# Performance work log

Measured on AMD Instinct MI355X. Metric: run time of the kernel, lower is better.

The kernel has to match this reference:

```python
import jax, jax.numpy as jnp
import numpy as np

B, S, D, H = 2, 1024, 1024, 16
DK, DV = 64, 64
E, F, K = 8, 2048, 2
FSH = 2 * F  # n_shared_experts * moe_inter_dim


def layernorm(x, w, eps=1e-8):
    # RMSNormLayer actually calls F.layer_norm(x, [dim], weight, None, eps)
    mu = jnp.mean(x, axis=-1, keepdims=True)
    var = jnp.mean((x - mu) ** 2, axis=-1, keepdims=True)
    return (x - mu) * jax.lax.rsqrt(var + eps) * w


def _forward(start_pos, x, mask, pos_embedding, attn_norm_w, ffn_norm_w,
             wq, bq, wk, bk, wv, bv, wo, bo, gate_w, gate_b,
             ew1, eb1, ew2, eb2, ew3, eb3, sw1, sb1, sw2, sb2, sw3, sb3):
    b, s, d = x.shape
    # --- attention sublayer ---
    xn = layernorm(x, attn_norm_w)
    q = (xn @ wq + bq).reshape(b, s, H, DK)
    k = (xn @ wk + bk).reshape(b, s, H, DK)
    v = (xn @ wv + bv).reshape(b, s, H, DV)
    score = jnp.einsum('bshk,bShk->bhsS', q, k) / np.float32(np.sqrt(DK))
    pe = pos_embedding[:, start_pos:start_pos + s, start_pos:start_pos + s]  # [H,s,s]
    score = score + pe[None, :, :, :] + mask[:s, :s]
    attn = jax.nn.softmax(score, axis=-1)
    o = jnp.einsum('bhsS,bShv->bshv', attn, v).reshape(b, s, H * DV)
    x = x + o @ wo + bo
    # --- MoE sublayer (eval-path math: y[t] = sum_k w[t,k]*expert_{idx[t,k]}(x[t])) ---
    hn = layernorm(x, ffn_norm_w)
    flat = hn.reshape(-1, d)  # [T, D]
    logits = flat @ gate_w.T + gate_b
    scores = jax.nn.softmax(logits, axis=-1)
    topk_w, topk_idx = jax.lax.top_k(scores, K)
    topk_w = topk_w / (jnp.sum(topk_w, axis=-1, keepdims=True) + 1e-20)
    # per-token per-expert combine weight [T, E]
    comb = jnp.sum(jax.nn.one_hot(topk_idx, E, dtype=flat.dtype) * topk_w[..., None], axis=1)
    # all experts densely (small E), SwiGLU per expert
    a = jnp.einsum('td,edf->tef', flat, ew1) + eb1
    g = jnp.einsum('td,edf->tef', flat, ew3) + eb3
    mid = jax.nn.silu(a) * g
    ye = jnp.einsum('tef,efd->ted', mid, ew2) + eb2  # [T, E, D]
    y = jnp.einsum('te,ted->td', comb, ye)
    # shared experts MLP on the normed input
    shared = (jax.nn.silu(flat @ sw1 + sb1) * (flat @ sw3 + sb3)) @ sw2 + sb2
    return x + (y + shared).reshape(b, s, d)


def setup_inputs() -> dict:
    key = jax.random.key(0)
    ks = jax.random.split(key, 16)
    def rn(i, shape, s=0.02):
        return jax.random.normal(ks[i], shape, jnp.float32) * s
    return dict(
        x=rn(0, (B, S, D), 1.0),
        start_pos=0,
        mask=jnp.zeros((S, S), jnp.float32),
        pos_embedding=rn(1, (H, S, S)),
        attn_norm_w=jnp.ones((D,), jnp.float32),
        ffn_norm_w=jnp.ones((D,), jnp.float32),
        wq=rn(2, (D, H * DK)), bq=jnp.zeros((H * DK,), jnp.float32),
        wk=rn(3, (D, H * DK)), bk=jnp.zeros((H * DK,), jnp.float32),
        wv=rn(4, (D, H * DV)), bv=jnp.zeros((H * DV,), jnp.float32),
        wo=rn(5, (H * DV, D)), bo=jnp.zeros((D,), jnp.float32),
        gate_w=rn(6, (E, D), 1.0), gate_b=rn(7, (E,), 1.0),
        ew1=rn(8, (E, D, F)), eb1=jnp.zeros((E, F), jnp.float32),
        ew2=rn(9, (E, F, D)), eb2=jnp.zeros((E, D), jnp.float32),
        ew3=rn(10, (E, D, F)), eb3=jnp.zeros((E, F), jnp.float32),
        sw1=rn(11, (D, FSH)), sb1=jnp.zeros((FSH,), jnp.float32),
        sw2=rn(12, (FSH, D)), sb2=jnp.zeros((D,), jnp.float32),
        sw3=rn(13, (D, FSH)), sb3=jnp.zeros((FSH,), jnp.float32),
    )


def reference(x, start_pos, mask, pos_embedding, attn_norm_w, ffn_norm_w,
              wq, bq, wk, bk, wv, bv, wo, bo, gate_w, gate_b,
              ew1, eb1, ew2, eb2, ew3, eb3, sw1, sb1, sw2, sb2, sw3, sb3):
    return _forward(start_pos, x, mask, pos_embedding, attn_norm_w, ffn_norm_w,
                    wq, bq, wk, bk, wv, bv, wo, bo, gate_w, gate_b,
                    ew1, eb1, ew2, eb2, ew3, eb3, sw1, sb1, sw2, sb2, sw3, sb3)
```

## Files before the change

### kernel.cpp

```cpp
#include <hip/hip_runtime.h>
#include <hip/hip_bf16.h>

#define BB 2
#define SS 1024
#define DD 1024
#define HH 16
#define DKV 64
#define EE 8
#define FF 2048
#define FSH2 4096

typedef __attribute__((ext_vector_type(8))) short bf16x8;
typedef __attribute__((ext_vector_type(4))) float f32x4;

#define EPI_PLAIN 0
#define EPI_SCATTER 2
#define AM_DENSE 0
#define AM_GATHER 1
#define AM_GROUP 2

__device__ inline unsigned pack_bf2(float lo, float hi) {
    __hip_bfloat162 h = __float22bfloat162_rn(float2{lo, hi});
    union { __hip_bfloat162 h2; unsigned u; } c; c.h2 = h; return c.u;
}
__device__ inline unsigned short bf16_1(float x) {
    union { __hip_bfloat16 b; unsigned short u; } c;
    c.b = __float2bfloat16(x); return c.u;
}

#define LOADT(s, k0) {                                                        \
    const float4* ap4 = (const float4*)(Ap + (k0));                           \
    pa##s##_0 = ap4[0]; pa##s##_1 = ap4[1];                                   \
    pa##s##_2 = ap4[2]; pa##s##_3 = ap4[3];                                   \
    const float* wp = Wcol + (size_t)((k0) + kg * 8) * N;                     \
    _Pragma("unroll")                                                         \
    for (int j = 0; j < 8; ++j) pb##s[j] = wp[(size_t)j * N];                 \
}
#define STAGET(s) {                                                           \
    uint4 aw0, aw1;                                                           \
    aw0.x = pack_bf2(pa##s##_0.x, pa##s##_0.y);                               \
    aw0.y = pack_bf2(pa##s##_0.z, pa##s##_0.w);                               \
    aw0.z = pack_bf2(pa##s##_1.x, pa##s##_1.y);                               \
    aw0.w = pack_bf2(pa##s##_1.z, pa##s##_1.w);                               \
    aw1.x = pack_bf2(pa##s##_2.x, pa##s##_2.y);                               \
    aw1.y = pack_bf2(pa##s##_2.z, pa##s##_2.w);                               \
    aw1.z = pack_bf2(pa##s##_3.x, pa##s##_3.y);                               \
    aw1.w = pack_bf2(pa##s##_3.z, pa##s##_3.w);                               \
    *(uint4*)&As[ar * 40 + ac] = aw0;                                         \
    *(uint4*)&As[ar * 40 + ac + 8] = aw1;                                     \
    uint4 bw;                                                                 \
    bw.x = pack_bf2(pb##s[0], pb##s[1]);  bw.y = pack_bf2(pb##s[2], pb##s[3]);\
    bw.z = pack_bf2(pb##s[4], pb##s[5]);  bw.w = pack_bf2(pb##s[6], pb##s[7]);\
    *(uint4*)&Bs[bn * 32 + slB * 8] = bw;                                     \
}
#define MFMAT() {                                                             \
    bf16x8 af[4], bfr[2];                                                     \
    _Pragma("unroll")                                                         \
    for (int m = 0; m < 4; ++m) {                                             \
        int row = wr * 64 + m * 16 + ll;                                      \
        af[m] = *(const bf16x8*)&As[row * 40 + lh * 8];                       \
    }                                                                         \
    _Pragma("unroll")                                                         \
    for (int n = 0; n < 2; ++n) {                                             \
        int col = wc * 32 + n * 16 + ll;                                      \
        int slot = lh ^ (col & 3);                                            \
        bfr[n] = *(const bf16x8*)&Bs[col * 32 + slot * 8];                    \
    }                                                                         \
    _Pragma("unroll")                                                         \
    for (int m = 0; m < 4; ++m)                                               \
        _Pragma("unroll")                                                     \
        for (int n = 0; n < 2; ++n)                                           \
            acc[m][n] = __builtin_amdgcn_mfma_f32_16x16x32_bf16(af[m], bfr[n], acc[m][n], 0, 0, 0); \
}
#define PHASET(s, nx) {                                                       \
    STAGET(s)                                                                 \
    if ((nx) < NT) LOADT(s, (nx) << 5)                                        \
    asm volatile("s_waitcnt lgkmcnt(0)\n\ts_barrier" ::: "memory");           \
    MFMAT()                                                                   \
    asm volatile("s_barrier" ::: "memory");                                   \
}

template<int EPI, int AMODE, int NSEL, int SPLITK>
__global__ __launch_bounds__(256, 2) void mgemm(
    const float* __restrict__ A,
    const float* __restrict__ W0, const float* __restrict__ W1p, const float* __restrict__ W2p,
    const float* __restrict__ b0, const float* __restrict__ b1p, const float* __restrict__ b2p,
    const float* __restrict__ addsrc,
    float* __restrict__ C0, float* __restrict__ C1p, float* __restrict__ C2p,
    int M, int N, int K,
    const int* __restrict__ tok_list, const int* __restrict__ cnt,
    const int* __restrict__ offs, const float* __restrict__ comb,
    const int* __restrict__ idx0, float* __restrict__ y1)
{
    __shared__ __align__(16) unsigned short As[128 * 40];
    __shared__ __align__(16) unsigned short Bs[64 * 32];
    __shared__ int rows_s[128];
    const int t = threadIdx.x;
    const float* W = W0; const float* bias = b0; float* C = C0;
    if (NSEL == 3) {
        if (blockIdx.z == 1) { W = W1p; bias = b1p; C = C1p; }
        else if (blockIdx.z == 2) { W = W2p; bias = b2p; C = C2p; }
    }
    const int e = (AMODE != AM_DENSE) ? blockIdx.z : 0;
    int ne = M, base = 0;
    if (AMODE != AM_DENSE) {
        ne = cnt[e];
        base = offs[e];
        if ((int)blockIdx.y * 128 >= ne) return;
        W += (size_t)e * K * N;
        bias += (size_t)e * N;
    }
    const int m0 = blockIdx.y * 128;
    const int n0 = blockIdx.x * 64;
    if (AMODE == AM_GATHER) {
        if (t < 128) {
            int li = m0 + t; if (li >= ne) li = ne - 1;
            rows_s[t] = tok_list[e * 2048 + li];
        }
        __syncthreads();
    }
    const int ar = t >> 1;
    const int ac = (t & 1) * 16;
    const int bn = t & 63;
    const int kg = t >> 6;
    const int slB = kg ^ (bn & 3);
    long arow;
    if (AMODE == AM_DENSE) arow = m0 + ar;
    else if (AMODE == AM_GATHER) arow = rows_s[ar];
    else { int li = m0 + ar; if (li >= ne) li = ne - 1; arow = base + li; }
    const int Kc = (SPLITK > 1) ? (K / SPLITK) : K;
    const size_t koff = (SPLITK > 1) ? (size_t)blockIdx.z * Kc : 0;
    const float* Ap = A + (size_t)arow * K + ac + koff;
    const float* Wcol = W + koff * N + n0 + bn;
    const int l = t & 63, w = t >> 6;
    const int wr = w >> 1, wc = w & 1;
    const int lh = l >> 4, ll = l & 15;
    f32x4 acc[4][2];
#pragma unroll
    for (int i = 0; i < 4; ++i)
#pragma unroll
        for (int j = 0; j < 2; ++j) acc[i][j] = f32x4{0.f, 0.f, 0.f, 0.f};

    const int NT = Kc >> 5;
    float4 pa0_0, pa0_1, pa0_2, pa0_3; float pb0[8];
    float4 pa1_0, pa1_1, pa1_2, pa1_3; float pb1[8];
    float4 pa2_0, pa2_1, pa2_2, pa2_3; float pb2[8];
    float4 pa3_0, pa3_1, pa3_2, pa3_3; float pb3[8];
    LOADT(0, 0)
    LOADT(1, 32)
    LOADT(2, 64)
    LOADT(3, 96)
    for (int it = 0; it < NT; it += 4) {
        PHASET(0, it + 4)
        PHASET(1, it + 5)
        PHASET(2, it + 6)
        PHASET(3, it + 7)
    }

#pragma unroll
    for (int m = 0; m < 4; ++m) {
#pragma unroll
        for (int n = 0; n < 2; ++n) {
            int colg = n0 + wc * 32 + n * 16 + ll;
            float bvv = (SPLITK > 1) ? 0.f : bias[colg];
#pragma unroll
            for (int j = 0; j < 4; ++j) {
                int li = m0 + wr * 64 + m * 16 + lh * 4 + j;
                float v = acc[m][n][j] + bvv;
                if (SPLITK > 1) {
                    C[(size_t)blockIdx.z * M * N + (size_t)li * N + colg] = v;
                } else if (EPI == EPI_PLAIN) {
                    if (AMODE == AM_DENSE) {
                        if (addsrc) v += addsrc[(size_t)li * N + colg];
                        C[(size_t)li * N + colg] = v;
                    } else {
                        if (li < ne) C[(size_t)(base + li) * N + colg] = v;
                    }
                } else {
                    if (li < ne) {
                        int tok = tok_list[e * 2048 + li];
                        float wgt = comb[tok * 8 + e];
                        float* dst = (idx0[tok] == e) ? C : y1;
                        dst[(size_t)tok * N + colg] = wgt * v;
                    }
                }
            }
        }
    }
}

#define LOAD2T(s, k0) {                                                       \
    const float4* ap4 = (const float4*)(Ap + (k0));                           \
    pa##s##_0 = ap4[0]; pa##s##_1 = ap4[1];                                   \
    pa##s##_2 = ap4[2]; pa##s##_3 = ap4[3];                                   \
    const float* wp1 = W1col + (size_t)((k0) + kg * 8) * N;                   \
    const float* wp3 = W3col + (size_t)((k0) + kg * 8) * N;                   \
    _Pragma("unroll")                                                         \
    for (int j = 0; j < 8; ++j) {                                             \
        pb1##s[j] = wp1[(size_t)j * N];                                       \
        pb3##s[j] = wp3[(size_t)j * N];                                       \
    }                                                                         \
}
#define STAGE2T(s) {                                                          \
    uint4 aw0, aw1;                                                           \
    aw0.x = pack_bf2(pa##s##_0.x, pa##s##_0.y);                               \
    aw0.y = pack_bf2(pa##s##_0.z, pa##s##_0.w);                               \
    aw0.z = pack_bf2(pa##s##_1.x, pa##s##_1.y);                               \
    aw0.w = pack_bf2(pa##s##_1.z, pa##s##_1.w);                               \
    aw1.x = pack_bf2(pa##s##_2.x, pa##s##_2.y);                               \
    aw1.y = pack_bf2(pa##s##_2.z, pa##s##_2.w);                               \
    aw1.z = pack_bf2(pa##s##_3.x, pa##s##_3.y);                               \
    aw1.w = pack_bf2(pa##s##_3.z, pa##s##_3.w);                               \
    *(uint4*)&As[ar * 40 + ac] = aw0;                                         \
    *(uint4*)&As[ar * 40 + ac + 8] = aw1;                                     \
    uint4 bw;                                                                 \
    bw.x = pack_bf2(pb1##s[0], pb1##s[1]);  bw.y = pack_bf2(pb1##s[2], pb1##s[3]); \
    bw.z = pack_bf2(pb1##s[4], pb1##s[5]);  bw.w = pack_bf2(pb1##s[6], pb1##s[7]); \
    *(uint4*)&B1s[bn * 32 + slB * 8] = bw;                                    \
    bw.x = pack_bf2(pb3##s[0], pb3##s[1]);  bw.y = pack_bf2(pb3##s[2], pb3##s[3]); \
    bw.z = pack_bf2(pb3##s[4], pb3##s[5]);  bw.w = pack_bf2(pb3##s[6], pb3##s[7]); \
    *(uint4*)&B3s[bn * 32 + slB * 8] = bw;                                    \
}
#define MFMA2T() {                                                            \
    bf16x8 af[4], bfr[2];                                                     \
    _Pragma("unroll")                                                         \
    for (int m = 0; m < 4; ++m) {                                             \
        int row = wr * 64 + m * 16 + ll;                                      \
        af[m] = *(const bf16x8*)&As[row * 40 + lh * 8];                       \
    }                                                                         \
    _Pragma("unroll")                                                         \
    for (int n = 0; n < 2; ++n) {                                             \
        int col = wc * 32 + n * 16 + ll;                                      \
        int slot = lh ^ (col & 3);                                            \
        bfr[n] = *(const bf16x8*)&B1s[col * 32 + slot * 8];                   \
    }                                                                         \
    _Pragma("unroll")                                                         \
    for (int m = 0; m < 4; ++m)                                               \
        _Pragma("unroll")                                                     \
        for (int n = 0; n < 2; ++n)                                           \
            acc1[m][n] = __builtin_amdgcn_mfma_f32_16x16x32_bf16(af[m], bfr[n], acc1[m][n], 0, 0, 0); \
    _Pragma("unroll")                                                         \
    for (int n = 0; n < 2; ++n) {                                             \
        int col = wc * 32 + n * 16 + ll;                                      \
        int slot = lh ^ (col & 3);                                            \
        bfr[n] = *(const bf16x8*)&B3s[col * 32 + slot * 8];                   \
    }                                                                         \
    _Pragma("unroll")                                                         \
    for (int m = 0; m < 4; ++m)                                               \
        _Pragma("unroll")                                                     \
        for (int n = 0; n < 2; ++n)                                           \
            acc3[m][n] = __builtin_amdgcn_mfma_f32_16x16x32_bf16(af[m], bfr[n], acc3[m][n], 0, 0, 0); \
}
#define PHASE2T(s, nx) {                                                      \
    STAGE2T(s)                                                                \
    if ((nx) < NT) LOAD2T(s, (nx) << 5)                                       \
    asm volatile("s_waitcnt lgkmcnt(0)\n\ts_barrier" ::: "memory");           \
    MFMA2T()                                                                  \
    asm volatile("s_barrier" ::: "memory");                                   \
}

#define MGEMM2_BODY(GATED) {                                                  \
    const int l = t & 63, w = t >> 6;                                         \
    const int wr = w >> 1, wc = w & 1;                                        \
    const int lh = l >> 4, ll = l & 15;                                       \
    f32x4 acc1[4][2], acc3[4][2];                                             \
    _Pragma("unroll")                                                         \
    for (int i = 0; i < 4; ++i)                                               \
        _Pragma("unroll")                                                     \
        for (int j = 0; j < 2; ++j) {                                         \
            acc1[i][j] = f32x4{0.f, 0.f, 0.f, 0.f};                           \
            acc3[i][j] = f32x4{0.f, 0.f, 0.f, 0.f};                           \
        }                                                                     \
    const int NT = K >> 5;                                                    \
    float4 pa0_0, pa0_1, pa0_2, pa0_3; float pb10[8], pb30[8];                \
    float4 pa1_0, pa1_1, pa1_2, pa1_3; float pb11[8], pb31[8];                \
    LOAD2T(0, 0)                                                              \
    LOAD2T(1, 32)                                                             \
    for (int it = 0; it < NT; it += 2) {                                      \
        PHASE2T(0, it + 2)                                                    \
        PHASE2T(1, it + 3)                                                    \
    }                                                                         \
    _Pragma("unroll")                                                         \
    for (int m = 0; m < 4; ++m) {                                             \
        _Pragma("unroll")                                                     \
        for (int n = 0; n < 2; ++n) {                                         \
            int colg = n0 + wc * 32 + n * 16 + ll;                            \
            float bv1 = b1[colg], bv3 = b3[colg];                             \
            _Pragma("unroll")                                                 \
            for (int j = 0; j < 4; ++j) {                                     \
                int li = m0 + wr * 64 + m * 16 + lh * 4 + j;                  \
                if (GATED && li >= ne) continue;                              \
                float a = acc1[m][n][j] + bv1;                                \
                float g = acc3[m][n][j] + bv3;                                \
                float sil = a / (1.0f + __expf(-a));                          \
                size_t off = (size_t)(base + li) * N + colg;                  \
                Out[off] = sil * g;                                           \
            }                                                                 \
        }                                                                     \
    }                                                                         \
}

template<int AMODE>
__global__ __launch_bounds__(256, 2) void mgemm2(
    const float* __restrict__ A,
    const float* __restrict__ W1, const float* __restrict__ W3,
    const float* __restrict__ B1, const float* __restrict__ B3,
    float* __restrict__ Out, int M, int N, int K,
    const int* __restrict__ tok_list, const int* __restrict__ cnt,
    const int* __restrict__ offs)
{
    __shared__ __align__(16) unsigned short As[128 * 40];
    __shared__ __align__(16) unsigned short B1s[64 * 32];
    __shared__ __align__(16) unsigned short B3s[64 * 32];
    __shared__ int rows_s[128];
    const int t = threadIdx.x;
    const int e = (AMODE == AM_GATHER) ? blockIdx.z : 0;
    int ne = M, base = 0;
    const float *w1 = W1, *w3 = W3, *b1 = B1, *b3 = B3;
    if (AMODE == AM_GATHER) {
        ne = cnt[e];
        base = offs[e];
        if ((int)blockIdx.y * 128 >= ne) return;
        w1 += (size_t)e * K * N; w3 += (size_t)e * K * N;
        b1 += (size_t)e * N;     b3 += (size_t)e * N;
    }
    const int m0 = blockIdx.y * 128;
    const int n0 = blockIdx.x * 64;
    if (AMODE == AM_GATHER) {
        if (t < 128) {
            int li = m0 + t; if (li >= ne) li = ne - 1;
            rows_s[t] = tok_list[e * 2048 + li];
        }
        __syncthreads();
    }
    const int ar = t >> 1;
    const int ac = (t & 1) * 16;
    const int bn = t & 63;
    const int kg = t >> 6;
    const int slB = kg ^ (bn & 3);
    long arow = (AMODE == AM_GATHER) ? (long)rows_s[ar] : (long)(m0 + ar);
    const float* Ap = A + (size_t)arow * K + ac;
    const float* W1col = w1 + n0 + bn;
    const float* W3col = w3 + n0 + bn;
    if (AMODE == AM_GATHER) { MGEMM2_BODY(1) } else { MGEMM2_BODY(0) }
}

__global__ __launch_bounds__(256, 2) void mgemm2m(
    const float* __restrict__ A,
    const float* __restrict__ W1r, const float* __restrict__ W3r,
    const float* __restrict__ B1r, const float* __restrict__ B3r,
    const float* __restrict__ W1sh, const float* __restrict__ W3sh,
    const float* __restrict__ B1sh, const float* __restrict__ B3sh,
    float* __restrict__ OutR, float* __restrict__ OutS, int K,
    const int* __restrict__ tok_list, const int* __restrict__ cnt,
    const int* __restrict__ offs)
{
    __shared__ __align__(16) unsigned short As[128 * 40];
    __shared__ __align__(16) unsigned short B1s[64 * 32];
    __shared__ __align__(16) unsigned short B3s[64 * 32];
    __shared__ int rows_s[128];
    const int t = threadIdx.x;
    const int z = blockIdx.z;
    const bool routed = (z < 8);
    int N, ne, base;
    const float *w1, *w3, *b1, *b3;
    float* Out;
    if (routed) {
        if ((int)blockIdx.x >= FF / 64) return;
        N = FF;
        ne = cnt[z];
        base = offs[z];
        if ((int)blockIdx.y * 128 >= ne) return;
        w1 = W1r + (size_t)z * K * N; w3 = W3r + (size_t)z * K * N;
        b1 = B1r + (size_t)z * N;     b3 = B3r + (size_t)z * N;
        Out = OutR;
    } else {
        N = FSH2;
        ne = 2048;
        base = 0;
        w1 = W1sh; w3 = W3sh; b1 = B1sh; b3 = B3sh;
        Out = OutS;
    }
    const int m0 = blockIdx.y * 128;
    const int n0 = blockIdx.x * 64;
    if (routed) {
        if (t < 128) {
            int li = m0 + t; if (li >= ne) li = ne - 1;
            rows_s[t] = tok_list[z * 2048 + li];
        }
        __syncthreads();
    }
    const int ar = t >> 1;
    const int ac = (t & 1) * 16;
    const int bn = t & 63;
    const int kg = t >> 6;
    const int slB = kg ^ (bn & 3);
    long arow = routed ? (long)rows_s[ar] : (long)(m0 + ar);
    const float* Ap = A + (size_t)arow * K + ac;
    const float* W1col = w1 + n0 + bn;
    const float* W3col = w3 + n0 + bn;
    if (routed) { MGEMM2_BODY(1) } else { MGEMM2_BODY(0) }
}

__global__ __launch_bounds__(256) void reducek(const float* __restrict__ P, int ns,
                                               const float* __restrict__ bias,
                                               const float* __restrict__ addsrc,
                                               float* __restrict__ out, int N) {
    size_t i = (size_t)blockIdx.x * 256 + threadIdx.x;
    const size_t MN4 = (size_t)2048 * N / 4;
    float4 s = ((const float4*)P)[i];
    for (int sl = 1; sl < ns; ++sl) {
        float4 p = ((const float4*)P)[i + (size_t)sl * MN4];
        s.x += p.x; s.y += p.y; s.z += p.z; s.w += p.w;
    }
    int col4 = (int)(i & ((N >> 2) - 1));
    float4 b = ((const float4*)bias)[col4];
    s.x += b.x; s.y += b.y; s.z += b.z; s.w += b.w;
    if (addsrc) {
        float4 a = ((const float4*)addsrc)[i];
        s.x += a.x; s.y += a.y; s.z += a.z; s.w += a.w;
    }
    ((float4*)out)[i] = s;
}

__global__ __launch_bounds__(256) void ln_kernel(const float* __restrict__ x,
                                                 const float* __restrict__ w,
                                                 float* __restrict__ y) {
    __shared__ float red[4], red2[4];
    const int row = blockIdx.x;
    const int t = threadIdx.x;
    const float4* xr = (const float4*)(x + (size_t)row * DD);
    float4 v = xr[t];
    float s = v.x + v.y + v.z + v.w;
    float q = v.x * v.x + v.y * v.y + v.z * v.z + v.w * v.w;
    for (int o = 32; o; o >>= 1) { s += __shfl_down(s, o); q += __shfl_down(q, o); }
    if ((t & 63) == 0) { red[t >> 6] = s; red2[t >> 6] = q; }
    __syncthreads();
    float S = red[0] + red[1] + red[2] + red[3];
    float Q = red2[0] + red2[1] + red2[2] + red2[3];
    float mu = S * (1.0f / DD);
    float var = Q * (1.0f / DD) - mu * mu;
    float inv = rsqrtf(var + 1e-8f);
    const float4* wr = (const float4*)w;
    float4 wv = wr[t];
    float4 o4;
    o4.x = (v.x - mu) * inv * wv.x;
    o4.y = (v.y - mu) * inv * wv.y;
    o4.z = (v.z - mu) * inv * wv.z;
    o4.w = (v.w - mu) * inv * wv.w;
    ((float4*)(y + (size_t)row * DD))[t] = o4;
}

__global__ __launch_bounds__(256) void attn_mfma(const float* __restrict__ Q,
                                                 const float* __restrict__ Kk,
                                                 const float* __restrict__ V,
                                                 const float* __restrict__ pe,
                                                 const float* __restrict__ mask,
                                                 const int* __restrict__ sp_ptr,
                                                 float* __restrict__ O) {
    __shared__ __align__(16) unsigned short Kt[64 * 64];
    __shared__ __align__(16) unsigned short Vt[64 * 64];
    __shared__ __align__(16) unsigned short Pl[4][16 * 64];
    const int t = threadIdx.x;
    const int w = t >> 6, l = t & 63;
    const int ll = l & 15, lh = l >> 4;
    const int bh = blockIdx.y;
    const int b = bh >> 4, h = bh & 15;
    const int q0 = blockIdx.x * 64;
    const int sp = sp_ptr[0];

    bf16x8 qf[2];
    {
        const float* qp = Q + (size_t)(b * SS + q0 + w * 16 + ll) * DD + h * 64 + lh * 8;
#pragma unroll
        for (int kk = 0; kk < 2; ++kk) {
            float4 x0 = *(const float4*)(qp + kk * 32);
            float4 x1 = *(const float4*)(qp + kk * 32 + 4);
            uint4 u;
            u.x = pack_bf2(x0.x * 0.125f, x0.y * 0.125f);
            u.y = pack_bf2(x0.z * 0.125f, x0.w * 0.125f);
            u.z = pack_bf2(x1.x * 0.125f, x1.y * 0.125f);
            u.w = pack_bf2(x1.z * 0.125f, x1.w * 0.125f);
            qf[kk] = *(bf16x8*)&u;
        }
    }
    f32x4 oacc[4];
#pragma unroll
    for (int n = 0; n < 4; ++n) oacc[n] = f32x4{0.f, 0.f, 0.f, 0.f};
    float mrun[4], lrun[4];
#pragma unroll
    for (int j = 0; j < 4; ++j) { mrun[j] = -3.0e38f; lrun[j] = 0.f; }

    const size_t pebase = (size_t)h * SS * SS + (size_t)sp;

    for (int kt0 = 0; kt0 < SS; kt0 += 64) {
        __syncthreads();
        {
            const int key = t >> 2, dg = (t & 3) * 16;
            const float* kp = Kk + (size_t)(b * SS + kt0 + key) * DD + h * 64 + dg;
            float4 k0 = *(const float4*)kp, k1 = *(const float4*)(kp + 4);
            float4 k2 = *(const float4*)(kp + 8), k3 = *(const float4*)(kp + 12);
            uint4 u0, u1;
            u0.x = pack_bf2(k0.x, k0.y); u0.y = pack_bf2(k0.z, k0.w);
            u0.z = pack_bf2(k1.x, k1.y); u0.w = pack_bf2(k1.z, k1.w);
            u1.x = pack_bf2(k2.x, k2.y); u1.y = pack_bf2(k2.z, k2.w);
            u1.z = pack_bf2(k3.x, k3.y); u1.w = pack_bf2(k3.z, k3.w);
            const int sw = (key & 7) << 4;
            *(uint4*)((char*)Kt + key * 128 + ((dg * 2) ^ sw)) = u0;
            *(uint4*)((char*)Kt + key * 128 + ((dg * 2 + 16) ^ sw)) = u1;
        }
        {
            const int kp2 = t & 31, vg = (t >> 5) * 8;
            const float* vp0 = V + (size_t)(b * SS + kt0 + 2 * kp2) * DD + h * 64 + vg;
            const float* vp1 = vp0 + DD;
            float4 a0 = *(const float4*)vp0, a1 = *(const float4*)(vp0 + 4);
            float4 b0 = *(const float4*)vp1, b1 = *(const float4*)(vp1 + 4);
            float va[8] = {a0.x, a0.y, a0.z, a0.w, a1.x, a1.y, a1.z, a1.w};
            float vb[8] = {b0.x, b0.y, b0.z, b0.w, b1.x, b1.y, b1.z, b1.w};
#pragma unroll
            for (int j = 0; j < 8; ++j) {
                int vd = vg + j;
                unsigned u = pack_bf2(va[j], vb[j]);
                *(unsigned*)((char*)Vt + vd * 128 + ((kp2 * 4) ^ ((vd & 7) << 4))) = u;
            }
        }
        __syncthreads();
        f32x4 sc[4];
#pragma unroll
        for (int n = 0; n < 4; ++n) sc[n] = f32x4{0.f, 0.f, 0.f, 0.f};
#pragma unroll
        for (int n = 0; n < 4; ++n) {
            const int key = n * 16 + ll;
            const int sw = (key & 7) << 4;
#pragma unroll
            for (int kk = 0; kk < 2; ++kk) {
                bf16x8 kf = *(const bf16x8*)((char*)Kt + key * 128 + ((kk * 64 + lh * 16) ^ sw));
                sc[n] = __builtin_amdgcn_mfma_f32_16x16x32_bf16(qf[kk], kf, sc[n], 0, 0, 0);
            }
        }
#pragma unroll
        for (int j = 0; j < 4; ++j) {
            const int qrow = q0 + w * 16 + lh * 4 + j;
            const float* per = pe + pebase + (size_t)(sp + qrow) * SS + kt0 + ll;
            const float* mar = mask + (size_t)qrow * SS + kt0 + ll;
#pragma unroll
            for (int n = 0; n < 4; ++n)
                sc[n][j] += per[n * 16] + mar[n * 16];
        }
#pragma unroll
        for (int j = 0; j < 4; ++j) {
            float mx = fmaxf(fmaxf(sc[0][j], sc[1][j]), fmaxf(sc[2][j], sc[3][j]));
#pragma unroll
            for (int o = 1; o < 16; o <<= 1) mx = fmaxf(mx, __shfl_xor(mx, o));
            float mnew = fmaxf(mrun[j], mx);
            float corr = __expf(mrun[j] - mnew);
            mrun[j] = mnew;
            float ssum = 0.f;
#pragma unroll
            for (int n = 0; n < 4; ++n) {
                float p = __expf(sc[n][j] - mnew);
                sc[n][j] = p;
                ssum += p;
            }
#pragma unroll
            for (int o = 1; o < 16; o <<= 1) ssum += __shfl_xor(ssum, o);
            lrun[j] = lrun[j] * corr + ssum;
#pragma unroll
            for (int n = 0; n < 4; ++n) oacc[n][j] *= corr;
        }
#pragma unroll
        for (int j = 0; j < 4; ++j) {
            const int lq = lh * 4 + j;
            const int sw = (lq & 7) << 4;
#pragma unroll
            for (int n = 0; n < 4; ++n) {
                const int key = n * 16 + ll;
                *(unsigned short*)((char*)Pl[w] + lq * 128 + ((key * 2) ^ sw)) =
                    bf16_1(sc[n][j]);
            }
        }
        asm volatile("s_waitcnt lgkmcnt(0)" ::: "memory");
        __builtin_amdgcn_sched_barrier(0);
#pragma unroll
        for (int kk = 0; kk < 2; ++kk) {
            const int lq = ll;
            bf16x8 pf = *(const bf16x8*)((char*)Pl[w] + lq * 128 +
                                         ((kk * 64 + lh * 16) ^ ((lq & 7) << 4)));
#pragma unroll
            for (int n = 0; n < 4; ++n) {
                const int vd = n * 16 + ll;
                bf16x8 vf = *(const bf16x8*)((char*)Vt + vd * 128 +
                                             ((kk * 64 + lh * 16) ^ ((vd & 7) << 4)));
                oacc[n] = __builtin_amdgcn_mfma_f32_16x16x32_bf16(pf, vf, oacc[n], 0, 0, 0);
            }
        }
    }
#pragma unroll
    for (int j = 0; j < 4; ++j) {
        const int qrow = q0 + w * 16 + lh * 4 + j;
        const float invl = 1.0f / lrun[j];
#pragma unroll
        for (int n = 0; n < 4; ++n)
            O[(size_t)(b * SS + qrow) * DD + h * 64 + n * 16 + ll] = oacc[n][j] * invl;
    }
}

__global__ __launch_bounds__(64) void gate_kernel(const float* __restrict__ hn,
                                                  const float* __restrict__ gw,
                                                  const float* __restrict__ gb,
                                                  float* __restrict__ comb,
                                                  int* __restrict__ idx0,
                                                  int* __restrict__ cnt,
                                                  int* __restrict__ tok_list) {
    __shared__ float lg[8];
    const int tok = blockIdx.x;
    const int lane = threadIdx.x;
    const int e = lane >> 3, chunk = lane & 7;
    const float* hr = hn + (size_t)tok * DD + chunk * 128;
    const float* gr = gw + (size_t)e * DD + chunk * 128;
    float p = 0.f;
    for (int j = 0; j < 128; ++j) p += hr[j] * gr[j];
    p += __shfl_down(p, 4, 8);
    p += __shfl_down(p, 2, 8);
    p += __shfl_down(p, 1, 8);
    if (chunk == 0) lg[e] = p + gb[e];
    __syncthreads();
    if (lane == 0) {
        float mx = lg[0];
        for (int i = 1; i < 8; ++i) mx = fmaxf(mx, lg[i]);
        float pr[8]; float ssum = 0.f;
        for (int i = 0; i < 8; ++i) { pr[i] = __expf(lg[i] - mx); ssum += pr[i]; }
        float is = 1.0f / ssum;
        for (int i = 0; i < 8; ++i) pr[i] *= is;
        int i1 = 0;
        for (int i = 1; i < 8; ++i) if (pr[i] > pr[i1]) i1 = i;
        int i2 = -1;
        for (int i = 0; i < 8; ++i) { if (i == i1) continue; if (i2 < 0 || pr[i] > pr[i2]) i2 = i; }
        float w0 = pr[i1], w1 = pr[i2];
        float nrm = 1.0f / (w0 + w1 + 1e-20f);
        w0 *= nrm; w1 *= nrm;
        for (int i = 0; i < 8; ++i) comb[tok * 8 + i] = 0.0f;
        comb[tok * 8 + i1] = w0;
        comb[tok * 8 + i2] = w1;
        idx0[tok] = i1;
        int s1 = atomicAdd(&cnt[i1], 1); tok_list[i1 * 2048 + s1] = tok;
        int s2 = atomicAdd(&cnt[i2], 1); tok_list[i2 * 2048 + s2] = tok;
    }
}

__global__ void init_cnt(int* cnt) { if (threadIdx.x < 8) cnt[threadIdx.x] = 0; }

__global__ void prefix_kernel(const int* __restrict__ cnt, int* __restrict__ offs) {
    if (threadIdx.x == 0) {
        int a = 0;
        for (int e = 0; e < 8; ++e) { offs[e] = a; a += cnt[e]; }
    }
}

__global__ __launch_bounds__(256) void final_kernel(const float* __restrict__ x2,
                                                    const float* __restrict__ y0,
                                                    const float* __restrict__ y1,
                                                    const float* __restrict__ sh,
                                                    float* __restrict__ out) {
    size_t i = (size_t)blockIdx.x * 256 + threadIdx.x;
    float4 a = ((const float4*)x2)[i];
    float4 b = ((const float4*)y0)[i];
    float4 c = ((const float4*)y1)[i];
    float4 d = ((const float4*)sh)[i];
    float4 o;
    o.x = a.x + b.x + c.x + d.x;
    o.y = a.y + b.y + c.y + d.y;
    o.z = a.z + b.z + c.z + d.z;
    o.w = a.w + b.w + c.w + d.w;
    ((float4*)out)[i] = o;
}

#define NUL6 nullptr, nullptr, nullptr, nullptr, nullptr, nullptr

extern "C" void kernel_launch(void* const* d_in, const int* in_sizes, int n_in,
                              void* d_out, int out_size, void* d_ws, size_t ws_size,
                              hipStream_t stream) {
    const float* x   = (const float*)d_in[0];
    const int*   sp  = (const int*)d_in[1];
    const float* mask= (const float*)d_in[2];
    const float* pe  = (const float*)d_in[3];
    const float* anw = (const float*)d_in[4];
    const float* fnw = (const float*)d_in[5];
    const float* wq  = (const float*)d_in[6];  const float* bq  = (const float*)d_in[7];
    const float* wk  = (const float*)d_in[8];  const float* bk  = (const float*)d_in[9];
    const float* wv  = (const float*)d_in[10]; const float* bv  = (const float*)d_in[11];
    const float* wo  = (const float*)d_in[12]; const float* bo  = (const float*)d_in[13];
    const float* gw  = (const float*)d_in[14]; const float* gb  = (const float*)d_in[15];
    const float* ew1 = (const float*)d_in[16]; const float* eb1 = (const float*)d_in[17];
    const float* ew2 = (const float*)d_in[18]; const float* eb2 = (const float*)d_in[19];
    const float* ew3 = (const float*)d_in[20]; const float* eb3 = (const float*)d_in[21];
    const float* sw1 = (const float*)d_in[22]; const float* sb1 = (const float*)d_in[23];
    const float* sw2 = (const float*)d_in[24]; const float* sb2 = (const float*)d_in[25];
    const float* sw3 = (const float*)d_in[26]; const float* sb3 = (const float*)d_in[27];

    float* ws = (float*)d_ws;
    const size_t M2 = (size_t)2048 * 1024;
    float* comb = ws;
    int* idx0   = (int*)(ws + 16384);
    int* cnt    = idx0 + 2048;
    int* offs   = cnt + 8;
    int* tok_list = offs + 8;
    float* base = ws + 65536;
    float* xn   = base;
    float* q    = base + 1 * M2;
    float* kbuf = base + 2 * M2;
    float* vbuf = base + 3 * M2;
    float* x2   = base + 4 * M2;
    float* amid = base + 5 * M2;
    float* smid = base + 9 * M2;
    const bool big = ws_size >= (size_t)(65536 + 13 * M2) * sizeof(float);
    float* o   = xn;
    float* hn  = q;
    float* y0  = xn;
    float* y1  = kbuf;
    float* sh  = vbuf;

    ln_kernel<<<2048, 256, 0, stream>>>(x, anw, xn);
    mgemm<EPI_PLAIN, AM_DENSE, 3, 1><<<dim3(16, 16, 3), 256, 0, stream>>>(
        xn, wq, wk, wv, bq, bk, bv, nullptr, q, kbuf, vbuf,
        2048, 1024, 1024, NUL6);
    attn_mfma<<<dim3(SS / 64, BB * HH), 256, 0, stream>>>(q, kbuf, vbuf, pe, mask, sp, o);
    mgemm<EPI_PLAIN, AM_DENSE, 1, 4><<<dim3(16, 16, 4), 256, 0, stream>>>(
        o, wo, nullptr, nullptr, bo, nullptr, nullptr, nullptr, amid, nullptr, nullptr,
        2048, 1024, 1024, NUL6);
    reducek<<<2048, 256, 0, stream>>>(amid, 4, bo, x, x2, 1024);
    ln_kernel<<<2048, 256, 0, stream>>>(x2, fnw, hn);
    init_cnt<<<1, 64, 0, stream>>>(cnt);
    gate_kernel<<<2048, 64, 0, stream>>>(hn, gw, gb, comb, idx0, cnt, tok_list);
    prefix_kernel<<<1, 64, 0, stream>>>(cnt, offs);

    if (big) {
        mgemm2m<<<dim3(64, 16, 9), 256, 0, stream>>>(
            hn, ew1, ew3, eb1, eb3, sw1, sw3, sb1, sb3,
            amid, smid, 1024, tok_list, cnt, offs);
        mgemm<EPI_SCATTER, AM_GROUP, 1, 1><<<dim3(16, 16, 8), 256, 0, stream>>>(
            amid, ew2, nullptr, nullptr, eb2, nullptr, nullptr, nullptr, y0, nullptr, nullptr,
            2048, DD, FF, tok_list, cnt, offs, comb, idx0, y1);
        mgemm<EPI_PLAIN, AM_DENSE, 1, 4><<<dim3(16, 16, 4), 256, 0, stream>>>(
            smid, sw2, nullptr, nullptr, sb2, nullptr, nullptr, nullptr, amid, nullptr, nullptr,
            2048, DD, FSH2, NUL6);
        reducek<<<2048, 256, 0, stream>>>(amid, 4, sb2, nullptr, sh, 1024);
    } else {
        mgemm2<AM_GATHER><<<dim3(32, 16, 8), 256, 0, stream>>>(
            hn, ew1, ew3, eb1, eb3, amid, 2048, FF, 1024, tok_list, cnt, offs);
        mgemm<EPI_SCATTER, AM_GROUP, 1, 1><<<dim3(16, 16, 8), 256, 0, stream>>>(
            amid, ew2, nullptr, nullptr, eb2, nullptr, nullptr, nullptr, y0, nullptr, nullptr,
            2048, DD, FF, tok_list, cnt, offs, comb, idx0, y1);
        mgemm2<AM_DENSE><<<dim3(64, 16), 256, 0, stream>>>(
            hn, sw1, sw3, sb1, sb3, amid, 2048, FSH2, 1024, nullptr, nullptr, nullptr);
        mgemm<EPI_PLAIN, AM_DENSE, 1, 1><<<dim3(16, 16), 256, 0, stream>>>(
            amid, sw2, nullptr, nullptr, sb2, nullptr, nullptr, nullptr, sh, nullptr, nullptr,
            2048, DD, FSH2, NUL6);
    }
    final_kernel<<<2048, 256, 0, stream>>>(x2, y0, y1, sh, (float*)d_out);
}
```

Baseline: 567.3 us.

## Fuse routed expert down-projection and shared-expert down-projection into one launch

Adds a kernel, mgemmF, that does both down-projection GEMMs in one grid. Slice z=0 computes the shared-expert W2 GEMM over the full K of 4096 with no split-K. Slices z=1..8 compute the routed-expert W2 GEMMs with the scatter and combine-weight epilogue. This removes two kernel launches and the split-K partial buffer plus its reduction pass, and lets the shared and routed work run on the GPU at the same time. The cost is that the shared slice uses only 256 blocks over a long K loop, so it may become the tail that finishes last.

Result: no change. 559.2 us (-1.4%).

```diff
diff --git a/kernel.cpp b/kernel.cpp
--- a/kernel.cpp
+++ b/kernel.cpp
@@ -181,6 +181,99 @@
                         int tok = tok_list[e * 2048 + li];
                         float wgt = comb[tok * 8 + e];
                         float* dst = (idx0[tok] == e) ? C : y1;
+                        dst[(size_t)tok * N + colg] = wgt * v;
+                    }
+                }
+            }
+        }
+    }
+}
+
+__global__ __launch_bounds__(256, 2) void mgemmF(
+    const float* __restrict__ Amid,
+    const float* __restrict__ Smid,
+    const float* __restrict__ W2r, const float* __restrict__ B2r,
+    const float* __restrict__ W2s, const float* __restrict__ B2s,
+    float* __restrict__ y0, float* __restrict__ y1, float* __restrict__ sh,
+    const int* __restrict__ tok_list, const int* __restrict__ cnt,
+    const int* __restrict__ offs, const float* __restrict__ comb,
+    const int* __restrict__ idx0)
+{
+    __shared__ __align__(16) unsigned short As[128 * 40];
+    __shared__ __align__(16) unsigned short Bs[64 * 32];
+    const int t = threadIdx.x;
+    const int z = blockIdx.z;
+    const bool sh_mode = (z == 0);
+    const int e = sh_mode ? 0 : (z - 1);
+    const int N = DD;
+    int K, ne, base;
+    const float *A, *W, *bias;
+    if (sh_mode) {
+        K = FSH2; ne = 2048; base = 0;
+        A = Smid; W = W2s; bias = B2s;
+    } else {
+        K = FF;
+        ne = cnt[e];
+        base = offs[e];
+        if ((int)blockIdx.y * 128 >= ne) return;
+        A = Amid;
+        W = W2r + (size_t)e * K * N;
+        bias = B2r + (size_t)e * N;
+    }
+    const int m0 = blockIdx.y * 128;
+    const int n0 = blockIdx.x * 64;
+    const int ar = t >> 1;
+    const int ac = (t & 1) * 16;
+    const int bn = t & 63;
+    const int kg = t >> 6;
+    const int slB = kg ^ (bn & 3);
+    long arow;
+    if (sh_mode) arow = m0 + ar;
+    else { int li = m0 + ar; if (li >= ne) li = ne - 1; arow = base + li; }
+    const float* Ap = A + (size_t)arow * K + ac;
+    const float* Wcol = W + n0 + bn;
+    const int l = t & 63, w = t >> 6;
+    const int wr = w >> 1, wc = w & 1;
+    const int lh = l >> 4, ll = l & 15;
+    f32x4 acc[4][2];
+#pragma unroll
+    for (int i = 0; i < 4; ++i)
+#pragma unroll
+        for (int j = 0; j < 2; ++j) acc[i][j] = f32x4{0.f, 0.f, 0.f, 0.f};
+
+    const int NT = K >> 5;
+    float4 pa0_0, pa0_1, pa0_2, pa0_3; float pb0[8];
+    float4 pa1_0, pa1_1, pa1_2, pa1_3; float pb1[8];
+    float4 pa2_0, pa2_1, pa2_2, pa2_3; float pb2[8];
+    float4 pa3_0, pa3_1, pa3_2, pa3_3; float pb3[8];
+    LOADT(0, 0)
+    LOADT(1, 32)
+    LOADT(2, 64)
+    LOADT(3, 96)
+    for (int it = 0; it < NT; it += 4) {
+        PHASET(0, it + 4)
+        PHASET(1, it + 5)
+        PHASET(2, it + 6)
+        PHASET(3, it + 7)
+    }
+
+#pragma unroll
+    for (int m = 0; m < 4; ++m) {
+#pragma unroll
+        for (int n = 0; n < 2; ++n) {
+            int colg = n0 + wc * 32 + n * 16 + ll;
+            float bvv = bias[colg];
+#pragma unroll
+            for (int j = 0; j < 4; ++j) {
+                int li = m0 + wr * 64 + m * 16 + lh * 4 + j;
+                float v = acc[m][n][j] + bvv;
+                if (sh_mode) {
+                    sh[(size_t)li * N + colg] = v;
+                } else {
+                    if (li < ne) {
+                        int tok = tok_list[e * 2048 + li];
+                        float wgt = comb[tok * 8 + e];
+                        float* dst = (idx0[tok] == e) ? y0 : y1;
                         dst[(size_t)tok * N + colg] = wgt * v;
                     }
                 }
@@ -738,13 +831,9 @@
         mgemm2m<<<dim3(64, 16, 9), 256, 0, stream>>>(
             hn, ew1, ew3, eb1, eb3, sw1, sw3, sb1, sb3,
             amid, smid, 1024, tok_list, cnt, offs);
-        mgemm<EPI_SCATTER, AM_GROUP, 1, 1><<<dim3(16, 16, 8), 256, 0, stream>>>(
-            amid, ew2, nullptr, nullptr, eb2, nullptr, nullptr, nullptr, y0, nullptr, nullptr,
-            2048, DD, FF, tok_list, cnt, offs, comb, idx0, y1);
-        mgemm<EPI_PLAIN, AM_DENSE, 1, 4><<<dim3(16, 16, 4), 256, 0, stream>>>(
-            smid, sw2, nullptr, nullptr, sb2, nullptr, nullptr, nullptr, amid, nullptr, nullptr,
-            2048, DD, FSH2, NUL6);
-        reducek<<<2048, 256, 0, stream>>>(amid, 4, sb2, nullptr, sh, 1024);
+        mgemmF<<<dim3(16, 16, 9), 256, 0, stream>>>(
+            amid, smid, ew2, eb2, sw2, sb2, y0, y1, sh,
+            tok_list, cnt, offs, comb, idx0);
     } else {
         mgemm2<AM_GATHER><<<dim3(32, 16, 8), 256, 0, stream>>>(
             hn, ew1, ew3, eb1, eb3, amid, 2048, FF, 1024, tok_list, cnt, offs);
```
